# Optimization experiments

Hardware: AMD Instinct MI355X
Metric: run time of the kernel (lower is better)

## Reference

```python
import jax, jax.numpy as jnp
import numpy as np

BATCH = 32768
TEXT_DIM = 384
HIDDEN = 256
NUM_LAYERS = 4
NUM_VERTS = 12
K_NN = 6


def _build_template():
    """Icosphere vertices (12, normalized) and row-normalized kNN adjacency (12,12)."""
    phi = (1.0 + 5.0 ** 0.5) / 2.0
    v = np.array([
        [-1, phi, 0], [1, phi, 0], [-1, -phi, 0], [1, -phi, 0],
        [0, -1, phi], [0, 1, phi], [0, -1, -phi], [0, 1, -phi],
        [phi, 0, -1], [phi, 0, 1], [-phi, 0, -1], [-phi, 0, 1],
    ], dtype=np.float32)
    v = v / np.linalg.norm(v, axis=1, keepdims=True)
    dist = np.linalg.norm(v[:, None, :] - v[None, :, :], axis=-1)  # (12,12)
    # k+1 smallest per row; index 0 is self (distance 0), skip it
    idx = np.argsort(dist, axis=1, kind='stable')[:, 1:K_NN + 1]
    adj = np.zeros((NUM_VERTS, NUM_VERTS), dtype=np.float32)
    rows = np.repeat(np.arange(NUM_VERTS), K_NN)
    adj[rows, idx.reshape(-1)] = 1.0
    adj = adj / (adj.sum(axis=1, keepdims=True) + 1e-6)
    return jnp.asarray(v), jnp.asarray(adj)


def setup_inputs() -> dict:
    key = jax.random.key(0)
    ks = jax.random.split(key, 8)
    template, adjacency = _build_template()
    scale = 0.02
    return {
        "text_emb": jax.random.normal(ks[0], (BATCH, TEXT_DIM), dtype=jnp.float32),
        "W_text": jax.random.normal(ks[1], (TEXT_DIM, HIDDEN), dtype=jnp.float32) * scale,
        "b_text": jnp.zeros((HIDDEN,), dtype=jnp.float32),
        "W_gnn": jax.random.normal(ks[2], (NUM_LAYERS, HIDDEN, HIDDEN), dtype=jnp.float32) * scale,
        "b_gnn": jnp.zeros((NUM_LAYERS, HIDDEN), dtype=jnp.float32),
        "W_out": jax.random.normal(ks[3], (HIDDEN, 3), dtype=jnp.float32) * scale,
        "b_out": jnp.zeros((3,), dtype=jnp.float32),
        "adjacency": adjacency,   # (12,12) buffer
        "template": template,     # (12,3) buffer
    }


def reference(text_emb, W_text, b_text, W_gnn, b_gnn, W_out, b_out, adjacency, template):
    # text projection -> broadcast to all nodes
    tf = text_emb @ W_text + b_text                       # (B, H)
    B = text_emb.shape[0]
    h = jnp.broadcast_to(tf[:, None, :], (B, NUM_VERTS, HIDDEN))
    # GNN layers: aggregate (shared adjacency across batch), project, relu
    for l in range(NUM_LAYERS):
        agg = jnp.einsum('nm,bmd->bnd', adjacency, h)     # (B, 12, H)
        h = jax.nn.relu(agg @ W_gnn[l] + b_gnn[l])
    displacements = h @ W_out + b_out                     # (B, 12, 3)
    return template[None, :, :] + displacements
```

## Files before the change

### kernel.cpp

```cpp
#include <hip/hip_runtime.h>
#include <stdint.h>

#define TD      384
#define HID     256

typedef __bf16 bf16;
typedef __attribute__((ext_vector_type(8))) __bf16 bf16x8;
typedef __attribute__((ext_vector_type(4))) float f32x4;

union FragU { uint4 u; bf16x8 f; };
union PackU { uint4 u; bf16 v[8]; };

__device__ inline f32x4 mfma16(bf16x8 a, bf16x8 b, f32x4 c) {
  return __builtin_amdgcn_mfma_f32_16x16x32_bf16(a, b, c, 0, 0, 0);
}

__global__ __launch_bounds__(256) void prep_wf(
    const float* __restrict__ W_text, const float* __restrict__ b_text,
    const float* __restrict__ W_gnn, const float* __restrict__ b_gnn,
    float* __restrict__ wf, float* __restrict__ bfv)
{
  int n = threadIdx.x;
  int k = blockIdx.x;
  const float* g0 = W_gnn;
  if (k < TD) {
    const float* trow = W_text + (size_t)k * HID;
    float a0 = 0.f, a1 = 0.f, a2 = 0.f, a3 = 0.f;
    for (int j = 0; j < HID; j += 4) {
      a0 += trow[j]     * g0[(j    ) * HID + n];
      a1 += trow[j + 1] * g0[(j + 1) * HID + n];
      a2 += trow[j + 2] * g0[(j + 2) * HID + n];
      a3 += trow[j + 3] * g0[(j + 3) * HID + n];
    }
    wf[(size_t)k * HID + n] = (a0 + a1) + (a2 + a3);
  } else {
    float a0 = 0.f, a1 = 0.f, a2 = 0.f, a3 = 0.f;
    for (int j = 0; j < HID; j += 4) {
      a0 += b_text[j]     * g0[(j    ) * HID + n];
      a1 += b_text[j + 1] * g0[(j + 1) * HID + n];
      a2 += b_text[j + 2] * g0[(j + 2) * HID + n];
      a3 += b_text[j + 3] * g0[(j + 3) * HID + n];
    }
    bfv[n] = (a0 + a1) + (a2 + a3) + b_gnn[n];
  }
}

__global__ __launch_bounds__(256) void prep_pack(
    const float* __restrict__ wf, const float* __restrict__ W_gnn,
    const float* __restrict__ W_out,
    bf16* __restrict__ wt_f, bf16* __restrict__ wt_g, float* __restrict__ wot)
{
  int bid = blockIdx.x, tid = threadIdx.x;
  if (bid < 48) {
    int idx = bid * 256 + tid;
    int cc = idx & 15, c = idx >> 4;
    int n16 = c / 48, oct = c - n16 * 48;
    int n = n16 * 16 + cc;
    PackU pk;
    #pragma unroll
    for (int j = 0; j < 8; j++) pk.v[j] = (bf16)wf[(oct * 8 + j) * HID + n];
    *(uint4*)(wt_f + idx * 8) = pk.u;
  } else if (bid < 144) {
    int idx = (bid - 48) * 256 + tid;
    int cc = idx & 15, c = idx >> 4;
    int l = c >> 9, c2 = c & 511;
    int oct = c2 & 31;
    int n = (c2 >> 5) * 16 + cc;
    const float* base = W_gnn + (size_t)(l + 1) * HID * HID;
    PackU pk;
    #pragma unroll
    for (int j = 0; j < 8; j++) pk.v[j] = (bf16)base[(oct * 8 + j) * HID + n];
    *(uint4*)(wt_g + idx * 8) = pk.u;
  } else {
    for (int t = tid; t < 3 * HID; t += 256) {
      int comp = t >> 8, k = t & 255;
      wot[comp * HID + k] = W_out[k * 3 + comp];
    }
  }
}

__global__ __launch_bounds__(512, 4) void mesh_kernel(
    const float* __restrict__ text,
    const bf16* __restrict__ wt_f,
    const bf16* __restrict__ wt_g,
    const float* __restrict__ b_f,
    const float* __restrict__ b_gnn,
    const float* __restrict__ wot,
    const float* __restrict__ b_out,
    const float* __restrict__ tmpl,
    float* __restrict__ out)
{
  __shared__ __align__(16) unsigned char smem[49920];
  unsigned char* Tbuf = smem;
  float* dispBuf = (float*)(smem + 49152);

  const int tid  = threadIdx.x;
  const int lane = tid & 63;
  const int w    = tid >> 6;
  const int cs   = w & 3;
  const int rh   = w >> 2;
  const int cc   = lane & 15;
  const int qq   = lane >> 4;
  const int rowbase = blockIdx.x * 64;

  f32x4 acc[2][4];

  auto zero_acc = [&]() {
    f32x4 z = {0.f, 0.f, 0.f, 0.f};
    #pragma unroll
    for (int mt = 0; mt < 2; mt++)
      #pragma unroll
      for (int nt = 0; nt < 4; nt++) acc[mt][nt] = z;
  };

  auto loadA = [&](int rowB, int ks, bf16x8* A) {
    #pragma unroll
    for (int mt = 0; mt < 2; mt++) {
      int m = rh * 32 + mt * 16 + cc;
      FragU fu;
      fu.u = *(const uint4*)(Tbuf + m * rowB + (((ks * 4 + qq) ^ (m & 7)) * 16));
      A[mt] = fu.f;
    }
  };

  auto loadB = [&](const char* wb, int K8, int ks, bf16x8* B) {
    #pragma unroll
    for (int nt = 0; nt < 4; nt++) {
      FragU fu;
      fu.u = *(const uint4*)(wb + (size_t)(nt * K8 + ks * 4) * 256);
      B[nt] = fu.f;
    }
  };

  auto epilogue = [&](const float* bias_ptr, bool relu) {
    float bias4[4];
    #pragma unroll
    for (int nt = 0; nt < 4; nt++) bias4[nt] = bias_ptr[cs * 64 + nt * 16 + cc];
    #pragma unroll
    for (int mt = 0; mt < 2; mt++) {
      #pragma unroll
      for (int nt = 0; nt < 4; nt++) {
        int col = cs * 64 + nt * 16 + cc;
        #pragma unroll
        for (int r = 0; r < 4; r++) {
          int m = rh * 32 + mt * 16 + qq * 4 + r;
          float v = acc[mt][nt][r] + bias4[nt];
          if (relu) v = fmaxf(v, 0.f);
          *(bf16*)(Tbuf + m * 512 + ((col >> 3) ^ (m & 7)) * 16 + (col & 7) * 2) = (bf16)v;
        }
      }
    }
  };

  const float* tbase = text + (size_t)rowbase * TD;
  auto stageHalf = [&](int half) {
    #pragma unroll
    for (int i = 0; i < 3; i++) {
      int id = i * 512 + tid;
      int m = id / 24, ol = id - m * 24;
      int o = half * 24 + ol;
      const float4* p = (const float4*)(tbase + m * TD + o * 8);
      float4 x = p[0], y = p[1];
      PackU pk;
      pk.v[0]=(bf16)x.x; pk.v[1]=(bf16)x.y; pk.v[2]=(bf16)x.z; pk.v[3]=(bf16)x.w;
      pk.v[4]=(bf16)y.x; pk.v[5]=(bf16)y.y; pk.v[6]=(bf16)y.z; pk.v[7]=(bf16)y.w;
      *(uint4*)(Tbuf + m * 768 + ((o ^ (m & 7)) * 16)) = pk.u;
    }
  };

  stageHalf(0);
  __syncthreads();
  stageHalf(1);
  zero_acc();
  const char* wbf = (const char*)wt_f + (size_t)(cs * 4 * 48 + qq) * 256 + cc * 16;
  {
    bf16x8 A[2], B[4], An[2], Bn[4];
    loadB(wbf, 48, 0, B);
    loadA(768, 0, A);
    #pragma unroll
    for (int ks = 0; ks < 6; ks++) {
      if (ks < 5) { loadB(wbf, 48, ks + 1, Bn); loadA(768, ks + 1, An); }
      #pragma unroll
      for (int mt = 0; mt < 2; mt++)
        #pragma unroll
        for (int nt = 0; nt < 4; nt++)
          acc[mt][nt] = mfma16(A[mt], B[nt], acc[mt][nt]);
      if (ks < 5) {
        #pragma unroll
        for (int t = 0; t < 2; t++) A[t] = An[t];
        #pragma unroll
        for (int t = 0; t < 4; t++) B[t] = Bn[t];
      }
    }
    __syncthreads();
    loadB(wbf, 48, 6, B);
    loadA(768, 6, A);
    #pragma unroll
    for (int ks = 6; ks < 12; ks++) {
      if (ks < 11) { loadB(wbf, 48, ks + 1, Bn); loadA(768, ks + 1, An); }
      #pragma unroll
      for (int mt = 0; mt < 2; mt++)
        #pragma unroll
        for (int nt = 0; nt < 4; nt++)
          acc[mt][nt] = mfma16(A[mt], B[nt], acc[mt][nt]);
      if (ks < 11) {
        #pragma unroll
        for (int t = 0; t < 2; t++) A[t] = An[t];
        #pragma unroll
        for (int t = 0; t < 4; t++) B[t] = Bn[t];
      }
    }
  }
  __syncthreads();
  epilogue(b_f, true);
  __syncthreads();

  for (int l = 0; l < 3; l++) {
    const char* wb = (const char*)wt_g + (size_t)l * HID * HID * 2
                   + (size_t)(cs * 4 * 32 + qq) * 256 + cc * 16;
    zero_acc();
    bf16x8 A[2], B[4], An[2], Bn[4];
    loadB(wb, 32, 0, B);
    loadA(512, 0, A);
    #pragma unroll
    for (int ks = 0; ks < 8; ks++) {
      if (ks < 7) { loadB(wb, 32, ks + 1, Bn); loadA(512, ks + 1, An); }
      #pragma unroll
      for (int mt = 0; mt < 2; mt++)
        #pragma unroll
        for (int nt = 0; nt < 4; nt++)
          acc[mt][nt] = mfma16(A[mt], B[nt], acc[mt][nt]);
      if (ks < 7) {
        #pragma unroll
        for (int t = 0; t < 2; t++) A[t] = An[t];
        #pragma unroll
        for (int t = 0; t < 4; t++) B[t] = Bn[t];
      }
    }
    __syncthreads();
    epilogue(b_gnn + (l + 1) * HID, true);
    __syncthreads();
  }

  if (tid < 192) {
    int comp = tid >> 6;
    int r = tid & 63;
    const float4* wrow = (const float4*)(wot + comp * HID);
    float s = 0.f;
    #pragma unroll 4
    for (int o = 0; o < 32; o++) {
      FragU fu; fu.u = *(const uint4*)(Tbuf + r * 512 + ((o ^ (r & 7)) * 16));
      float4 w0 = wrow[2 * o], w1 = wrow[2 * o + 1];
      s += (float)fu.f[0]*w0.x + (float)fu.f[1]*w0.y + (float)fu.f[2]*w0.z + (float)fu.f[3]*w0.w;
      s += (float)fu.f[4]*w1.x + (float)fu.f[5]*w1.y + (float)fu.f[6]*w1.z + (float)fu.f[7]*w1.w;
    }
    dispBuf[r * 3 + comp] = s + b_out[comp];
  }
  __syncthreads();

  #pragma unroll
  for (int ii = 0; ii < 5; ii++) {
    int i = ii * 512 + tid;
    if (i < 2304) {
      int row = i / 36;
      int j = i - row * 36;
      out[(size_t)rowbase * 36 + i] = tmpl[j] + dispBuf[row * 3 + j % 3];
    }
  }
}

extern "C" void kernel_launch(void* const* d_in, const int* in_sizes, int n_in,
                              void* d_out, int out_size, void* d_ws, size_t ws_size,
                              hipStream_t stream) {
  const float* text   = (const float*)d_in[0];
  const float* W_text = (const float*)d_in[1];
  const float* b_text = (const float*)d_in[2];
  const float* W_gnn  = (const float*)d_in[3];
  const float* b_gnn  = (const float*)d_in[4];
  const float* W_out  = (const float*)d_in[5];
  const float* b_out  = (const float*)d_in[6];
  const float* tmpl   = (const float*)d_in[8];
  float* outp = (float*)d_out;

  float* wf   = (float*)d_ws;
  float* bfv  = wf + TD * HID;
  float* wot  = bfv + HID;
  bf16* wt_f  = (bf16*)(wot + 3 * HID);
  bf16* wt_g  = wt_f + TD * HID;

  prep_wf<<<TD + 1, 256, 0, stream>>>(W_text, b_text, W_gnn, b_gnn, wf, bfv);
  prep_pack<<<145, 256, 0, stream>>>(wf, W_gnn, W_out, wt_f, wt_g, wot);
  mesh_kernel<<<32768 / 64, 512, 0, stream>>>(text, wt_f, wt_g, bfv, b_gnn,
                                              wot, b_out, tmpl, outp);
}
```

Measured before the change: 144.2 us.

## Retile mesh GEMMs per wave, ping-pong activations, deepen B prefetch

The main kernel changes its wave tiling. Each of the 8 waves now covers all 64 rows and a 32-column slice instead of a 32x64 tile. Activations move through two shared-memory buffers, so the barrier before each epilogue write goes away, and the B fragments are prefetched two k-steps ahead, with MFMA issue wrapped in s_setprio. The weight-folding prep kernel now computes 8 output rows per block to reuse each W_gnn load. The cost is 80KB of LDS per block, which may lower occupancy below the 4 blocks/CU hint, plus more A-fragment LDS reads per wave.

```diff
diff --git a/kernel.cpp b/kernel.cpp
--- a/kernel.cpp
+++ b/kernel.cpp
@@ -21,27 +21,22 @@
     float* __restrict__ wf, float* __restrict__ bfv)
 {
   int n = threadIdx.x;
-  int k = blockIdx.x;
   const float* g0 = W_gnn;
-  if (k < TD) {
-    const float* trow = W_text + (size_t)k * HID;
-    float a0 = 0.f, a1 = 0.f, a2 = 0.f, a3 = 0.f;
-    for (int j = 0; j < HID; j += 4) {
-      a0 += trow[j]     * g0[(j    ) * HID + n];
-      a1 += trow[j + 1] * g0[(j + 1) * HID + n];
-      a2 += trow[j + 2] * g0[(j + 2) * HID + n];
-      a3 += trow[j + 3] * g0[(j + 3) * HID + n];
-    }
-    wf[(size_t)k * HID + n] = (a0 + a1) + (a2 + a3);
+  if (blockIdx.x < 48) {
+    int k0 = blockIdx.x * 8;
+    float a[8] = {0.f,0.f,0.f,0.f,0.f,0.f,0.f,0.f};
+    for (int j = 0; j < HID; j++) {
+      float g = g0[(size_t)j * HID + n];
+      #pragma unroll
+      for (int r = 0; r < 8; r++)
+        a[r] += W_text[(size_t)(k0 + r) * HID + j] * g;
+    }
+    #pragma unroll
+    for (int r = 0; r < 8; r++) wf[(size_t)(k0 + r) * HID + n] = a[r];
   } else {
-    float a0 = 0.f, a1 = 0.f, a2 = 0.f, a3 = 0.f;
-    for (int j = 0; j < HID; j += 4) {
-      a0 += b_text[j]     * g0[(j    ) * HID + n];
-      a1 += b_text[j + 1] * g0[(j + 1) * HID + n];
-      a2 += b_text[j + 2] * g0[(j + 2) * HID + n];
-      a3 += b_text[j + 3] * g0[(j + 3) * HID + n];
-    }
-    bfv[n] = (a0 + a1) + (a2 + a3) + b_gnn[n];
+    float s = 0.f;
+    for (int j = 0; j < HID; j++) s += b_text[j] * g0[(size_t)j * HID + n];
+    bfv[n] = s + b_gnn[n];
   }
 }
 
@@ -90,63 +85,73 @@
     const float* __restrict__ tmpl,
     float* __restrict__ out)
 {
-  __shared__ __align__(16) unsigned char smem[49920];
+  __shared__ __align__(16) unsigned char smem[81920];
   unsigned char* Tbuf = smem;
-  float* dispBuf = (float*)(smem + 49152);
+  unsigned char* Ha   = smem;
+  unsigned char* Hb   = smem + 49152;
+  float* dispBuf = (float*)(smem + 32768);
 
   const int tid  = threadIdx.x;
   const int lane = tid & 63;
-  const int w    = tid >> 6;
-  const int cs   = w & 3;
-  const int rh   = w >> 2;
+  const int cs   = tid >> 6;
   const int cc   = lane & 15;
   const int qq   = lane >> 4;
   const int rowbase = blockIdx.x * 64;
 
-  f32x4 acc[2][4];
+  f32x4 acc[4][2];
 
   auto zero_acc = [&]() {
     f32x4 z = {0.f, 0.f, 0.f, 0.f};
     #pragma unroll
-    for (int mt = 0; mt < 2; mt++)
-      #pragma unroll
-      for (int nt = 0; nt < 4; nt++) acc[mt][nt] = z;
-  };
-
-  auto loadA = [&](int rowB, int ks, bf16x8* A) {
-    #pragma unroll
-    for (int mt = 0; mt < 2; mt++) {
-      int m = rh * 32 + mt * 16 + cc;
+    for (int mt = 0; mt < 4; mt++)
+      #pragma unroll
+      for (int nt = 0; nt < 2; nt++) acc[mt][nt] = z;
+  };
+
+  auto loadA = [&](const unsigned char* src, int rowB, int ks, bf16x8* A) {
+    #pragma unroll
+    for (int mt = 0; mt < 4; mt++) {
+      int m = mt * 16 + cc;
       FragU fu;
-      fu.u = *(const uint4*)(Tbuf + m * rowB + (((ks * 4 + qq) ^ (m & 7)) * 16));
+      fu.u = *(const uint4*)(src + m * rowB + (((ks * 4 + qq) ^ (m & 7)) * 16));
       A[mt] = fu.f;
     }
   };
 
   auto loadB = [&](const char* wb, int K8, int ks, bf16x8* B) {
     #pragma unroll
-    for (int nt = 0; nt < 4; nt++) {
+    for (int nt = 0; nt < 2; nt++) {
       FragU fu;
       fu.u = *(const uint4*)(wb + (size_t)(nt * K8 + ks * 4) * 256);
       B[nt] = fu.f;
     }
   };
 
-  auto epilogue = [&](const float* bias_ptr, bool relu) {
-    float bias4[4];
-    #pragma unroll
-    for (int nt = 0; nt < 4; nt++) bias4[nt] = bias_ptr[cs * 64 + nt * 16 + cc];
-    #pragma unroll
-    for (int mt = 0; mt < 2; mt++) {
-      #pragma unroll
-      for (int nt = 0; nt < 4; nt++) {
-        int col = cs * 64 + nt * 16 + cc;
+  auto mmac = [&](bf16x8* A, bf16x8* B) {
+    __builtin_amdgcn_s_setprio(1);
+    #pragma unroll
+    for (int mt = 0; mt < 4; mt++)
+      #pragma unroll
+      for (int nt = 0; nt < 2; nt++)
+        acc[mt][nt] = mfma16(A[mt], B[nt], acc[mt][nt]);
+    __builtin_amdgcn_s_setprio(0);
+  };
+
+  auto epilogue = [&](unsigned char* dst, const float* bias_ptr, bool relu) {
+    float bias2[2];
+    #pragma unroll
+    for (int nt = 0; nt < 2; nt++) bias2[nt] = bias_ptr[cs * 32 + nt * 16 + cc];
+    #pragma unroll
+    for (int mt = 0; mt < 4; mt++) {
+      #pragma unroll
+      for (int nt = 0; nt < 2; nt++) {
+        int col = cs * 32 + nt * 16 + cc;
         #pragma unroll
         for (int r = 0; r < 4; r++) {
-          int m = rh * 32 + mt * 16 + qq * 4 + r;
-          float v = acc[mt][nt][r] + bias4[nt];
+          int m = mt * 16 + qq * 4 + r;
+          float v = acc[mt][nt][r] + bias2[nt];
           if (relu) v = fmaxf(v, 0.f);
-          *(bf16*)(Tbuf + m * 512 + ((col >> 3) ^ (m & 7)) * 16 + (col & 7) * 2) = (bf16)v;
+          *(bf16*)(dst + m * 512 + ((col >> 3) ^ (m & 7)) * 16 + (col & 7) * 2) = (bf16)v;
         }
       }
     }
@@ -171,74 +176,76 @@
   stageHalf(0);
   __syncthreads();
   stageHalf(1);
+
   zero_acc();
-  const char* wbf = (const char*)wt_f + (size_t)(cs * 4 * 48 + qq) * 256 + cc * 16;
+  const char* wbf = (const char*)wt_f + (size_t)(cs * 2 * 48 + qq) * 256 + cc * 16;
   {
-    bf16x8 A[2], B[4], An[2], Bn[4];
-    loadB(wbf, 48, 0, B);
-    loadA(768, 0, A);
+    bf16x8 A[4], An[4], B0[2], B1[2], Bt[2];
+    loadB(wbf, 48, 0, B0);
+    loadB(wbf, 48, 1, B1);
+    loadA(Tbuf, 768, 0, A);
     #pragma unroll
     for (int ks = 0; ks < 6; ks++) {
-      if (ks < 5) { loadB(wbf, 48, ks + 1, Bn); loadA(768, ks + 1, An); }
-      #pragma unroll
-      for (int mt = 0; mt < 2; mt++)
-        #pragma unroll
-        for (int nt = 0; nt < 4; nt++)
-          acc[mt][nt] = mfma16(A[mt], B[nt], acc[mt][nt]);
+      loadB(wbf, 48, ks + 2, Bt);
+      if (ks < 5) loadA(Tbuf, 768, ks + 1, An);
+      mmac(A, B0);
+      #pragma unroll
+      for (int t = 0; t < 2; t++) { B0[t] = B1[t]; B1[t] = Bt[t]; }
       if (ks < 5) {
         #pragma unroll
-        for (int t = 0; t < 2; t++) A[t] = An[t];
-        #pragma unroll
-        for (int t = 0; t < 4; t++) B[t] = Bn[t];
+        for (int t = 0; t < 4; t++) A[t] = An[t];
       }
     }
     __syncthreads();
-    loadB(wbf, 48, 6, B);
-    loadA(768, 6, A);
+    loadA(Tbuf, 768, 6, A);
     #pragma unroll
     for (int ks = 6; ks < 12; ks++) {
-      if (ks < 11) { loadB(wbf, 48, ks + 1, Bn); loadA(768, ks + 1, An); }
-      #pragma unroll
-      for (int mt = 0; mt < 2; mt++)
-        #pragma unroll
-        for (int nt = 0; nt < 4; nt++)
-          acc[mt][nt] = mfma16(A[mt], B[nt], acc[mt][nt]);
+      if (ks < 10) loadB(wbf, 48, ks + 2, Bt);
+      if (ks < 11) loadA(Tbuf, 768, ks + 1, An);
+      mmac(A, B0);
+      #pragma unroll
+      for (int t = 0; t < 2; t++) B0[t] = B1[t];
+      if (ks < 10) {
+        #pragma unroll
+        for (int t = 0; t < 2; t++) B1[t] = Bt[t];
+      }
       if (ks < 11) {
         #pragma unroll
-        for (int t = 0; t < 2; t++) A[t] = An[t];
-        #pragma unroll
-        for (int t = 0; t < 4; t++) B[t] = Bn[t];
-      }
-    }
-  }
+        for (int t = 0; t < 4; t++) A[t] = An[t];
+      }
+    }
+  }
+  epilogue(Hb, b_f, true);
   __syncthreads();
-  epilogue(b_f, true);
-  __syncthreads();
-
+
+  #pragma unroll
   for (int l = 0; l < 3; l++) {
+    const unsigned char* src = (l & 1) ? Ha : Hb;
+    unsigned char*       dst = (l & 1) ? Hb : Ha;
     const char* wb = (const char*)wt_g + (size_t)l * HID * HID * 2
-                   + (size_t)(cs * 4 * 32 + qq) * 256 + cc * 16;
+                   + (size_t)(cs * 2 * 32 + qq) * 256 + cc * 16;
     zero_acc();
-    bf16x8 A[2], B[4], An[2], Bn[4];
-    loadB(wb, 32, 0, B);
-    loadA(512, 0, A);
+    bf16x8 A[4], An[4], B0[2], B1[2], Bt[2];
+    loadB(wb, 32, 0, B0);
+    loadB(wb, 32, 1, B1);
+    loadA(src, 512, 0, A);
     #pragma unroll
     for (int ks = 0; ks < 8; ks++) {
-      if (ks < 7) { loadB(wb, 32, ks + 1, Bn); loadA(512, ks + 1, An); }
-      #pragma unroll
-      for (int mt = 0; mt < 2; mt++)
-        #pragma unroll
-        for (int nt = 0; nt < 4; nt++)
-          acc[mt][nt] = mfma16(A[mt], B[nt], acc[mt][nt]);
+      if (ks < 6) loadB(wb, 32, ks + 2, Bt);
+      if (ks < 7) loadA(src, 512, ks + 1, An);
+      mmac(A, B0);
+      #pragma unroll
+      for (int t = 0; t < 2; t++) B0[t] = B1[t];
+      if (ks < 6) {
+        #pragma unroll
+        for (int t = 0; t < 2; t++) B1[t] = Bt[t];
+      }
       if (ks < 7) {
         #pragma unroll
-        for (int t = 0; t < 2; t++) A[t] = An[t];
-        #pragma unroll
-        for (int t = 0; t < 4; t++) B[t] = Bn[t];
-      }
-    }
-    __syncthreads();
-    epilogue(b_gnn + (l + 1) * HID, true);
+        for (int t = 0; t < 4; t++) A[t] = An[t];
+      }
+    }
+    epilogue(dst, b_gnn + (l + 1) * HID, true);
     __syncthreads();
   }
 
@@ -249,7 +256,7 @@
     float s = 0.f;
     #pragma unroll 4
     for (int o = 0; o < 32; o++) {
-      FragU fu; fu.u = *(const uint4*)(Tbuf + r * 512 + ((o ^ (r & 7)) * 16));
+      FragU fu; fu.u = *(const uint4*)(Ha + r * 512 + ((o ^ (r & 7)) * 16));
       float4 w0 = wrow[2 * o], w1 = wrow[2 * o + 1];
       s += (float)fu.f[0]*w0.x + (float)fu.f[1]*w0.y + (float)fu.f[2]*w0.z + (float)fu.f[3]*w0.w;
       s += (float)fu.f[4]*w1.x + (float)fu.f[5]*w1.y + (float)fu.f[6]*w1.z + (float)fu.f[7]*w1.w;
@@ -288,7 +295,7 @@
   bf16* wt_f  = (bf16*)(wot + 3 * HID);
   bf16* wt_g  = wt_f + TD * HID;
 
-  prep_wf<<<TD + 1, 256, 0, stream>>>(W_text, b_text, W_gnn, b_gnn, wf, bfv);
+  prep_wf<<<49, 256, 0, stream>>>(W_text, b_text, W_gnn, b_gnn, wf, bfv);
   prep_pack<<<145, 256, 0, stream>>>(wf, W_gnn, W_out, wt_f, wt_g, wot);
   mesh_kernel<<<32768 / 64, 512, 0, stream>>>(text, wt_f, wt_g, bfv, b_gnn,
                                               wot, b_out, tmpl, outp);
```

Measured after the change: 171.5 us. 18.9% more time.
